# Performance work log

Hardware: AMD Instinct MI355X
Metric: run time of the kernel (lower is better)

Reference implementation:

```python
import jax, jax.numpy as jnp
import numpy as np

B, C, H, W = 8, 192, 64, 64
RED = 8
CR = C // RED  # 24


def prelu(x, a):
    # a is a single shared slope (PyTorch nn.PReLU() default num_parameters=1)
    return jnp.where(x >= 0, x, a * x)


def conv1x1(x, w, b):
    # x: [B,C,H,W], w: [O,C], b: [O] -> [B,O,H,W]
    return jnp.einsum('bchw,oc->bohw', x, w) + b[None, :, None, None]


def setup_inputs() -> dict:
    key = jax.random.key(0)
    ks = jax.random.split(key, 7)
    scale1 = 1.0 / np.sqrt(C)
    return {
        'x': jax.random.normal(ks[0], (B, C, H, W), dtype=jnp.float32),
        'w1': jax.random.uniform(ks[1], (CR, C), jnp.float32, -scale1, scale1),
        'b1': jnp.zeros((CR,), jnp.float32),
        'a1': jnp.full((1,), 0.25, jnp.float32),
        'w2': jax.random.uniform(ks[2], (CR, C), jnp.float32, -scale1, scale1),
        'b2': jnp.zeros((CR,), jnp.float32),
        'a2': jnp.full((1,), 0.25, jnp.float32),
        'wa': jax.random.uniform(ks[3], (C, C), jnp.float32, -scale1, scale1),
        'ba': jnp.zeros((C,), jnp.float32),
        'aa': jnp.full((1,), 0.25, jnp.float32),
    }


def reference(x, w1, b1, a1, w2, b2, a2, wa, ba, aa):
    b, c, h, w = x.shape
    hw = h * w
    q = prelu(conv1x1(x, w1, b1), a1)          # [B,Cr,H,W]
    k = prelu(conv1x1(x, w2, b2), a2)          # [B,Cr,H,W]
    v = prelu(conv1x1(x, wa, ba), aa)          # [B,C,H,W]
    q = q.reshape(b, -1, hw).transpose(0, 2, 1)   # [B,HW,Cr]
    k = k.reshape(b, -1, hw)                      # [B,Cr,HW]
    score = jax.nn.softmax(jnp.einsum('bnc,bcm->bnm', q, k), axis=2)  # [B,HW,HW]
    v = v.reshape(b, c, hw).transpose(0, 2, 1)    # [B,HW,C]
    out = jnp.einsum('bnm,bmc->bnc', score, v)    # [B,HW,C]
    return out.transpose(0, 2, 1).reshape(b, c, h, w)
```

## Files before the change

kernel.cpp:

```cpp
#include <hip/hip_runtime.h>
#include <hip/hip_fp16.h>

#define HW 4096
#define NC 192
#define NB 8
#define DQK 32
#define LOG2E 1.4426950408889634f
#define THRL 11.541560327f

typedef _Float16 f16x8 __attribute__((ext_vector_type(8)));
typedef float f32x4 __attribute__((ext_vector_type(4)));
typedef unsigned int u32x4 __attribute__((ext_vector_type(4)));

#define BAR() do { asm volatile("s_waitcnt lgkmcnt(0)" ::: "memory"); \
                   __builtin_amdgcn_s_barrier();                      \
                   asm volatile("" ::: "memory"); } while (0)

static __device__ __forceinline__ unsigned int pkrtz(float a, float b) {
  auto h = __builtin_amdgcn_cvt_pkrtz(a, b);
  return __builtin_bit_cast(unsigned int, h);
}
static __device__ __forceinline__ unsigned short f2h_bits(float f) {
  _Float16 h = (_Float16)f;
  union { _Float16 h; unsigned short u; } cv; cv.h = h; return cv.u;
}

__global__ void wtrans_kernel(
    const float* __restrict__ w1, const float* __restrict__ b1, const float* __restrict__ a1,
    const float* __restrict__ w2, const float* __restrict__ b2, const float* __restrict__ a2,
    const float* __restrict__ wa, const float* __restrict__ ba, const float* __restrict__ aa,
    float* __restrict__ wt)
{
  const int c = blockIdx.x;
  const int o = threadIdx.x;
  if (o >= 240) return;
  float v;
  if (c < 192) {
    if (o < 24)      v = w1[o * 192 + c];
    else if (o < 48) v = w2[(o - 24) * 192 + c];
    else             v = wa[(o - 48) * 192 + c];
  } else if (c == 192) {
    v = (o < 24) ? b1[o] : (o < 48) ? b2[o - 24] : ba[o - 48];
  } else {
    v = (o < 24) ? a1[0] : (o < 48) ? a2[0] : aa[0];
  }
  wt[c * 240 + o] = v;
}

__global__ __launch_bounds__(256) void proj_kernel(
    const float* __restrict__ x, const float* __restrict__ wt,
    unsigned short* __restrict__ Qn, unsigned short* __restrict__ Kn,
    unsigned short* __restrict__ Vt)
{
  const int g   = blockIdx.y;
  const int tid = threadIdx.x;
  const int bp  = (blockIdx.x * 256 + tid) * 2;
  const int b   = bp >> 12;
  const int pos = bp & (HW - 1);

  const float* xb = x + (size_t)b * NC * HW + pos;
  float acc0[16], acc1[16];
  #pragma unroll
  for (int o = 0; o < 16; ++o) { acc0[o] = 0.f; acc1[o] = 0.f; }

  #pragma unroll 4
  for (int c = 0; c < 192; ++c) {
    float2 xv = *reinterpret_cast<const float2*>(xb + (size_t)c * HW);
    const float* wr = wt + c * 240 + g * 16;
    #pragma unroll
    for (int o = 0; o < 16; ++o) {
      float w = wr[o];
      acc0[o] = fmaf(w, xv.x, acc0[o]);
      acc1[o] = fmaf(w, xv.y, acc1[o]);
    }
  }

  const float* brow = wt + 192 * 240 + g * 16;
  const float* srow = wt + 193 * 240 + g * 16;
  unsigned short h0[16], h1[16];
  #pragma unroll
  for (int o = 0; o < 16; ++o) {
    float bias = brow[o], sm1 = srow[o] - 1.f;
    float v0 = acc0[o] + bias; v0 += fminf(v0, 0.f) * sm1;
    float v1 = acc1[o] + bias; v1 += fminf(v1, 0.f) * sm1;
    if (g * 16 + o < 24) { v0 *= LOG2E; v1 *= LOG2E; }
    h0[o] = f2h_bits(v0);
    h1[o] = f2h_bits(v1);
  }

  if (g >= 3) {
    const int vch0 = g * 16 - 48;
    unsigned int* vp = reinterpret_cast<unsigned int*>(
        Vt + ((size_t)b * NC + vch0) * HW + pos);
    #pragma unroll
    for (int o = 0; o < 16; ++o)
      vp[o * (HW / 2)] = (unsigned int)h0[o] | ((unsigned int)h1[o] << 16);
  } else {
    u32x4 lo0, hi0, lo1, hi1;
    #pragma unroll
    for (int j = 0; j < 4; ++j) {
      lo0[j] = (unsigned int)h0[2 * j] | ((unsigned int)h0[2 * j + 1] << 16);
      hi0[j] = (unsigned int)h0[8 + 2 * j] | ((unsigned int)h0[9 + 2 * j] << 16);
      lo1[j] = (unsigned int)h1[2 * j] | ((unsigned int)h1[2 * j + 1] << 16);
      hi1[j] = (unsigned int)h1[8 + 2 * j] | ((unsigned int)h1[9 + 2 * j] << 16);
    }
    const size_t bpos = (size_t)b * HW + pos;
    if (g == 0) {
      u32x4* q0 = reinterpret_cast<u32x4*>(Qn + bpos * DQK);
      q0[0] = lo0; q0[1] = hi0;
      u32x4* q1 = reinterpret_cast<u32x4*>(Qn + (bpos + 1) * DQK);
      q1[0] = lo1; q1[1] = hi1;
    } else if (g == 1) {
      *reinterpret_cast<u32x4*>(Qn + bpos * DQK + 16) = lo0;
      *reinterpret_cast<u32x4*>(Kn + bpos * DQK) = hi0;
      *reinterpret_cast<u32x4*>(Qn + (bpos + 1) * DQK + 16) = lo1;
      *reinterpret_cast<u32x4*>(Kn + (bpos + 1) * DQK) = hi1;
    } else {
      u32x4* k0 = reinterpret_cast<u32x4*>(Kn + bpos * DQK + 8);
      k0[0] = lo0; k0[1] = hi0;
      u32x4* k1 = reinterpret_cast<u32x4*>(Kn + (bpos + 1) * DQK + 8);
      k1[0] = lo1; k1[1] = hi1;
    }
  }
}

__global__ __launch_bounds__(512, 4) void flash_kernel(
    const unsigned short* __restrict__ Qn, const unsigned short* __restrict__ Kn,
    const unsigned short* __restrict__ Vt, float* __restrict__ out)
{
  const int b    = blockIdx.y;
  const int q0   = blockIdx.x * 64;
  const int tid  = threadIdx.x;
  const int w    = tid >> 6;
  const int half = w >> 2;
  const int wi   = w & 3;
  const int lane = tid & 63;
  const int lq   = lane & 15;
  const int lk   = lane >> 4;

  __shared__ u32x4 Pex[2][2][4][2][64];
  __shared__ float alphaL[2][2][4][16];
  __shared__ float mlL[2][2][64];

  const int mbase = half * (HW / 2);
  const int sigb  = 8 * (lq >> 2) + (lq & 3);

  f16x8 qfrag = *reinterpret_cast<const f16x8*>(
      Qn + ((size_t)b * HW + q0 + 16 * wi + lq) * DQK + 8 * lk);

  float m = -1e30f;
  f32x4 O[12], lacc;
  #pragma unroll
  for (int i = 0; i < 12; ++i) O[i] = (f32x4){0.f, 0.f, 0.f, 0.f};
  lacc = (f32x4){0.f, 0.f, 0.f, 0.f};

  const unsigned short* Kb = Kn + (size_t)b * HW * DQK + (size_t)sigb * DQK + 8 * lk;
  const unsigned short* Vw = Vt + (size_t)b * NC * HW + (size_t)(wi * 48 + lq) * HW + 8 * lk;

  f16x8 vones;
  #pragma unroll
  for (int i = 0; i < 8; ++i) vones[i] = (_Float16)1.0f;

  f16x8 Kf[4];

  auto qk_softmax = [&](int par) {
    f32x4 s[4];
    #pragma unroll
    for (int t = 0; t < 4; ++t)
      s[t] = __builtin_amdgcn_mfma_f32_16x16x32_f16(Kf[t], qfrag,
              (f32x4){0.f, 0.f, 0.f, 0.f}, 0, 0, 0);
    float pmax = s[0][0];
    #pragma unroll
    for (int t = 0; t < 4; ++t)
      #pragma unroll
      for (int r = 0; r < 4; ++r) pmax = fmaxf(pmax, s[t][r]);
    float alpha = 1.f;
    if (__any(pmax > m + THRL)) {
      pmax = fmaxf(pmax, __shfl_xor(pmax, 16));
      pmax = fmaxf(pmax, __shfl_xor(pmax, 32));
      float mn = fmaxf(m, pmax);
      alpha = exp2f(m - mn);
      m = mn;
    }
    float pv[4][4];
    #pragma unroll
    for (int t = 0; t < 4; ++t)
      #pragma unroll
      for (int r = 0; r < 4; ++r) pv[t][r] = exp2f(s[t][r] - m);
    u32x4 pa0, pa1;
    pa0[0] = pkrtz(pv[0][0], pv[0][1]); pa0[1] = pkrtz(pv[0][2], pv[0][3]);
    pa0[2] = pkrtz(pv[2][0], pv[2][1]); pa0[3] = pkrtz(pv[2][2], pv[2][3]);
    pa1[0] = pkrtz(pv[1][0], pv[1][1]); pa1[1] = pkrtz(pv[1][2], pv[1][3]);
    pa1[2] = pkrtz(pv[3][0], pv[3][1]); pa1[3] = pkrtz(pv[3][2], pv[3][3]);
    Pex[par][half][wi][0][lane] = pa0;
    Pex[par][half][wi][1][lane] = pa1;
    if (lane < 16) alphaL[par][half][wi][lane] = alpha;
  };

  #pragma unroll
  for (int t = 0; t < 4; ++t)
    Kf[t] = *reinterpret_cast<const f16x8*>(
        Kb + (size_t)(mbase + 32 * (t & 1) + 4 * (t >> 1)) * DQK);
  qk_softmax(0);
  BAR();

  const int NIT = HW / 2 / 64;
  for (int it = 0; it < NIT; ++it) {
    const int prt = it & 1;
    const bool notlast = (it + 1 < NIT);
    const int m0 = mbase + it * 64;
    const int mnext = m0 + 64;
    if (notlast) {
      #pragma unroll
      for (int t = 0; t < 4; ++t)
        Kf[t] = *reinterpret_cast<const f16x8*>(
            Kb + (size_t)(mnext + 32 * (t & 1) + 4 * (t >> 1)) * DQK);
    }
    #pragma unroll
    for (int tr = 0; tr < 4; ++tr) {
      f32x4 al = *reinterpret_cast<const f32x4*>(&alphaL[prt][half][tr][4 * lk]);
      int diff = (al[0] != 1.f) | (al[1] != 1.f) | (al[2] != 1.f) | (al[3] != 1.f);
      if (__any(diff)) {
        #pragma unroll
        for (int tc = 0; tc < 3; ++tc) {
          O[tr * 3 + tc][0] *= al[0]; O[tr * 3 + tc][1] *= al[1];
          O[tr * 3 + tc][2] *= al[2]; O[tr * 3 + tc][3] *= al[3];
        }
        if (tr == wi) {
          lacc[0] *= al[0]; lacc[1] *= al[1]; lacc[2] *= al[2]; lacc[3] *= al[3];
        }
      }
    }
    {
      f16x8 paf[4];
      #pragma unroll
      for (int tr = 0; tr < 4; ++tr)
        paf[tr] = __builtin_bit_cast(f16x8, Pex[prt][half][tr][0][lane]);
      f16x8 pw = __builtin_bit_cast(f16x8, Pex[prt][half][wi][0][lane]);
      lacc = __builtin_amdgcn_mfma_f32_16x16x32_f16(pw, vones, lacc, 0, 0, 0);
      #pragma unroll
      for (int tc = 0; tc < 3; ++tc) {
        f16x8 vb = *reinterpret_cast<const f16x8*>(
            Vw + (size_t)tc * 16 * HW + m0);
        #pragma unroll
        for (int tr = 0; tr < 4; ++tr)
          O[tr * 3 + tc] = __builtin_amdgcn_mfma_f32_16x16x32_f16(
              paf[tr], vb, O[tr * 3 + tc], 0, 0, 0);
      }
    }
    if (notlast) qk_softmax(prt ^ 1);
    {
      f16x8 paf[4];
      #pragma unroll
      for (int tr = 0; tr < 4; ++tr)
        paf[tr] = __builtin_bit_cast(f16x8, Pex[prt][half][tr][1][lane]);
      f16x8 pw = __builtin_bit_cast(f16x8, Pex[prt][half][wi][1][lane]);
      lacc = __builtin_amdgcn_mfma_f32_16x16x32_f16(pw, vones, lacc, 0, 0, 0);
      #pragma unroll
      for (int tc = 0; tc < 3; ++tc) {
        f16x8 vb = *reinterpret_cast<const f16x8*>(
            Vw + (size_t)tc * 16 * HW + m0 + 32);
        #pragma unroll
        for (int tr = 0; tr < 4; ++tr)
          O[tr * 3 + tc] = __builtin_amdgcn_mfma_f32_16x16x32_f16(
              paf[tr], vb, O[tr * 3 + tc], 0, 0, 0);
      }
    }
    BAR();
  }

  if (lane < 16) mlL[half][0][16 * wi + lane] = m;
  if (lq == 0) {
    #pragma unroll
    for (int r = 0; r < 4; ++r) mlL[half][1][16 * wi + 4 * lk + r] = lacc[r];
  }
  f32x4* Ost = reinterpret_cast<f32x4*>(&Pex[0][0][0][0][0]);
  if (half == 1) {
    #pragma unroll
    for (int i = 0; i < 8; ++i) Ost[(wi * 8 + i) * 64 + lane] = O[i];
  }
  BAR();
  f32x4 f0v[4], f1v[4];
  if (half == 0) {
    #pragma unroll
    for (int tr = 0; tr < 4; ++tr) {
      f32x4 m0v = *reinterpret_cast<const f32x4*>(&mlL[0][0][16 * tr + 4 * lk]);
      f32x4 l0v = *reinterpret_cast<const f32x4*>(&mlL[0][1][16 * tr + 4 * lk]);
      f32x4 m1v = *reinterpret_cast<const f32x4*>(&mlL[1][0][16 * tr + 4 * lk]);
      f32x4 l1v = *reinterpret_cast<const f32x4*>(&mlL[1][1][16 * tr + 4 * lk]);
      #pragma unroll
      for (int r = 0; r < 4; ++r) {
        float M  = fmaxf(m0v[r], m1v[r]);
        float s0 = exp2f(m0v[r] - M), s1 = exp2f(m1v[r] - M);
        float L  = s0 * l0v[r] + s1 * l1v[r];
        f0v[tr][r] = s0 / L; f1v[tr][r] = s1 / L;
      }
    }
    #pragma unroll
    for (int i = 0; i < 8; ++i) {
      const int tr = i / 3, tc = i - tr * 3;
      f32x4 o1 = Ost[(wi * 8 + i) * 64 + lane];
      f32x4 o;
      #pragma unroll
      for (int r = 0; r < 4; ++r) o[r] = O[i][r] * f0v[tr][r] + o1[r] * f1v[tr][r];
      *reinterpret_cast<f32x4*>(
          out + ((size_t)b * NC + wi * 48 + tc * 16 + lq) * HW + q0 + 16 * tr + 4 * lk) = o;
    }
  }
  BAR();
  if (half == 1) {
    #pragma unroll
    for (int i = 0; i < 4; ++i) Ost[(wi * 4 + i) * 64 + lane] = O[8 + i];
  }
  BAR();
  if (half == 0) {
    #pragma unroll
    for (int i = 8; i < 12; ++i) {
      const int tr = i / 3, tc = i - tr * 3;
      f32x4 o1 = Ost[(wi * 4 + (i - 8)) * 64 + lane];
      f32x4 o;
      #pragma unroll
      for (int r = 0; r < 4; ++r) o[r] = O[i][r] * f0v[tr][r] + o1[r] * f1v[tr][r];
      *reinterpret_cast<f32x4*>(
          out + ((size_t)b * NC + wi * 48 + tc * 16 + lq) * HW + q0 + 16 * tr + 4 * lk) = o;
    }
  }
}

extern "C" void kernel_launch(void* const* d_in, const int* in_sizes, int n_in,
                              void* d_out, int out_size, void* d_ws, size_t ws_size,
                              hipStream_t stream) {
  const float* x  = (const float*)d_in[0];
  const float* w1 = (const float*)d_in[1];
  const float* b1 = (const float*)d_in[2];
  const float* a1 = (const float*)d_in[3];
  const float* w2 = (const float*)d_in[4];
  const float* b2 = (const float*)d_in[5];
  const float* a2 = (const float*)d_in[6];
  const float* wa = (const float*)d_in[7];
  const float* ba = (const float*)d_in[8];
  const float* aa = (const float*)d_in[9];
  float* out = (float*)d_out;

  unsigned short* Qn = (unsigned short*)d_ws;
  unsigned short* Kn = Qn + (size_t)NB * HW * DQK;
  unsigned short* Vt = Kn + (size_t)NB * HW * DQK;
  float* wt = out + (out_size - 49152);

  (void)hipMemsetAsync(Qn, 0, (size_t)NB * HW * DQK * 2 * sizeof(unsigned short), stream);

  wtrans_kernel<<<dim3(194), 256, 0, stream>>>(w1, b1, a1, w2, b2, a2, wa, ba, aa, wt);

  dim3 pgrid(HW * NB / 512, 15);
  proj_kernel<<<pgrid, 256, 0, stream>>>(x, wt, Qn, Kn, Vt);

  dim3 fgrid(HW / 64, NB);
  flash_kernel<<<fgrid, 512, 0, stream>>>(Qn, Kn, Vt, out);
}
```

Baseline: 184.0 us.

## Halve flash block query tile and widen per-wave channel span with early V prefetch

Each flash-attention block now covers 32 queries with 256 threads instead of 64 queries with 512. Each wave covers 96 output channels across 2 query row tiles instead of 48 channels across 4, and the batch index is folded into a 1D grid of 1024 blocks. V fragments for the first half of each step are loaded before the K prefetch and rescale, to hide global load latency. The smaller tile gives more blocks for the CUs, but K and V are reused across fewer queries, so memory traffic rises. The projection kernel's position index is switched to a precomputed variable.

After: 363.2 us. 1.97x slower.

```diff
diff --git a/kernel.cpp b/kernel.cpp
--- a/kernel.cpp
+++ b/kernel.cpp
@@ -104,7 +104,7 @@
       lo1[j] = (unsigned int)h1[2 * j] | ((unsigned int)h1[2 * j + 1] << 16);
       hi1[j] = (unsigned int)h1[8 + 2 * j] | ((unsigned int)h1[9 + 2 * j] << 16);
     }
-    const size_t bpos = (size_t)b * HW + pos;
+    const size_t bpos = (size_t)bp;
     if (g == 0) {
       u32x4* q0 = reinterpret_cast<u32x4*>(Qn + bpos * DQK);
       q0[0] = lo0; q0[1] = hi0;
@@ -124,23 +124,23 @@
   }
 }
 
-__global__ __launch_bounds__(512, 4) void flash_kernel(
+__global__ __launch_bounds__(256, 4) void flash_kernel(
     const unsigned short* __restrict__ Qn, const unsigned short* __restrict__ Kn,
     const unsigned short* __restrict__ Vt, float* __restrict__ out)
 {
-  const int b    = blockIdx.y;
-  const int q0   = blockIdx.x * 64;
+  const int b    = blockIdx.x & 7;
+  const int q0   = (blockIdx.x >> 3) * 32;
   const int tid  = threadIdx.x;
   const int w    = tid >> 6;
-  const int half = w >> 2;
-  const int wi   = w & 3;
+  const int half = w >> 1;
+  const int wi   = w & 1;
   const int lane = tid & 63;
   const int lq   = lane & 15;
   const int lk   = lane >> 4;
 
-  __shared__ u32x4 Pex[2][2][4][2][64];
-  __shared__ float alphaL[2][2][4][16];
-  __shared__ float mlL[2][2][64];
+  __shared__ u32x4 Pex[2][2][2][2][64];
+  __shared__ float alphaL[2][2][2][16];
+  __shared__ float mlL[2][2][32];
 
   const int mbase = half * (HW / 2);
   const int sigb  = 8 * (lq >> 2) + (lq & 3);
@@ -155,7 +155,7 @@
   lacc = (f32x4){0.f, 0.f, 0.f, 0.f};
 
   const unsigned short* Kb = Kn + (size_t)b * HW * DQK + (size_t)sigb * DQK + 8 * lk;
-  const unsigned short* Vw = Vt + (size_t)b * NC * HW + (size_t)(wi * 48 + lq) * HW + 8 * lk;
+  const unsigned short* Vw = Vt + (size_t)b * NC * HW + (size_t)(wi * 96 + lq) * HW + 8 * lk;
 
   f16x8 vones;
   #pragma unroll
@@ -210,6 +210,10 @@
     const bool notlast = (it + 1 < NIT);
     const int m0 = mbase + it * 64;
     const int mnext = m0 + 64;
+    f16x8 vb0[6];
+    #pragma unroll
+    for (int tc = 0; tc < 6; ++tc)
+      vb0[tc] = *reinterpret_cast<const f16x8*>(Vw + (size_t)tc * 16 * HW + m0);
     if (notlast) {
       #pragma unroll
       for (int t = 0; t < 4; ++t)
@@ -217,14 +221,14 @@
             Kb + (size_t)(mnext + 32 * (t & 1) + 4 * (t >> 1)) * DQK);
     }
     #pragma unroll
-    for (int tr = 0; tr < 4; ++tr) {
+    for (int tr = 0; tr < 2; ++tr) {
       f32x4 al = *reinterpret_cast<const f32x4*>(&alphaL[prt][half][tr][4 * lk]);
       int diff = (al[0] != 1.f) | (al[1] != 1.f) | (al[2] != 1.f) | (al[3] != 1.f);
       if (__any(diff)) {
         #pragma unroll
-        for (int tc = 0; tc < 3; ++tc) {
-          O[tr * 3 + tc][0] *= al[0]; O[tr * 3 + tc][1] *= al[1];
-          O[tr * 3 + tc][2] *= al[2]; O[tr * 3 + tc][3] *= al[3];
+        for (int tc = 0; tc < 6; ++tc) {
+          O[tr * 6 + tc][0] *= al[0]; O[tr * 6 + tc][1] *= al[1];
+          O[tr * 6 + tc][2] *= al[2]; O[tr * 6 + tc][3] *= al[3];
         }
         if (tr == wi) {
           lacc[0] *= al[0]; lacc[1] *= al[1]; lacc[2] *= al[2]; lacc[3] *= al[3];
@@ -232,38 +236,43 @@
       }
     }
     {
-      f16x8 paf[4];
-      #pragma unroll
-      for (int tr = 0; tr < 4; ++tr)
+      f16x8 paf[2];
+      #pragma unroll
+      for (int tr = 0; tr < 2; ++tr)
         paf[tr] = __builtin_bit_cast(f16x8, Pex[prt][half][tr][0][lane]);
-      f16x8 pw = __builtin_bit_cast(f16x8, Pex[prt][half][wi][0][lane]);
-      lacc = __builtin_amdgcn_mfma_f32_16x16x32_f16(pw, vones, lacc, 0, 0, 0);
-      #pragma unroll
-      for (int tc = 0; tc < 3; ++tc) {
-        f16x8 vb = *reinterpret_cast<const f16x8*>(
-            Vw + (size_t)tc * 16 * HW + m0);
+      lacc = __builtin_amdgcn_mfma_f32_16x16x32_f16(paf[wi], vones, lacc, 0, 0, 0);
+      #pragma unroll
+      for (int tc = 0; tc < 6; ++tc)
         #pragma unroll
-        for (int tr = 0; tr < 4; ++tr)
-          O[tr * 3 + tc] = __builtin_amdgcn_mfma_f32_16x16x32_f16(
-              paf[tr], vb, O[tr * 3 + tc], 0, 0, 0);
-      }
-    }
+        for (int tr = 0; tr < 2; ++tr)
+          O[tr * 6 + tc] = __builtin_amdgcn_mfma_f32_16x16x32_f16(
+              paf[tr], vb0[tc], O[tr * 6 + tc], 0, 0, 0);
+    }
+    f16x8 vb1a[3];
+    #pragma unroll
+    for (int tc = 0; tc < 3; ++tc)
+      vb1a[tc] = *reinterpret_cast<const f16x8*>(Vw + (size_t)tc * 16 * HW + m0 + 32);
     if (notlast) qk_softmax(prt ^ 1);
     {
-      f16x8 paf[4];
-      #pragma unroll
-      for (int tr = 0; tr < 4; ++tr)
+      f16x8 paf[2];
+      #pragma unroll
+      for (int tr = 0; tr < 2; ++tr)
         paf[tr] = __builtin_bit_cast(f16x8, Pex[prt][half][tr][1][lane]);
-      f16x8 pw = __builtin_bit_cast(f16x8, Pex[prt][half][wi][1][lane]);
-      lacc = __builtin_amdgcn_mfma_f32_16x16x32_f16(pw, vones, lacc, 0, 0, 0);
-      #pragma unroll
-      for (int tc = 0; tc < 3; ++tc) {
+      lacc = __builtin_amdgcn_mfma_f32_16x16x32_f16(paf[wi], vones, lacc, 0, 0, 0);
+      #pragma unroll
+      for (int tc = 0; tc < 3; ++tc)
+        #pragma unroll
+        for (int tr = 0; tr < 2; ++tr)
+          O[tr * 6 + tc] = __builtin_amdgcn_mfma_f32_16x16x32_f16(
+              paf[tr], vb1a[tc], O[tr * 6 + tc], 0, 0, 0);
+      #pragma unroll
+      for (int tc = 3; tc < 6; ++tc) {
         f16x8 vb = *reinterpret_cast<const f16x8*>(
             Vw + (size_t)tc * 16 * HW + m0 + 32);
         #pragma unroll
-        for (int tr = 0; tr < 4; ++tr)
-          O[tr * 3 + tc] = __builtin_amdgcn_mfma_f32_16x16x32_f16(
-              paf[tr], vb, O[tr * 3 + tc], 0, 0, 0);
+        for (int tr = 0; tr < 2; ++tr)
+          O[tr * 6 + tc] = __builtin_amdgcn_mfma_f32_16x16x32_f16(
+              paf[tr], vb, O[tr * 6 + tc], 0, 0, 0);
       }
     }
     BAR();
@@ -277,13 +286,13 @@
   f32x4* Ost = reinterpret_cast<f32x4*>(&Pex[0][0][0][0][0]);
   if (half == 1) {
     #pragma unroll
-    for (int i = 0; i < 8; ++i) Ost[(wi * 8 + i) * 64 + lane] = O[i];
+    for (int i = 0; i < 6; ++i) Ost[(wi * 6 + i) * 64 + lane] = O[i];
   }
   BAR();
-  f32x4 f0v[4], f1v[4];
+  f32x4 f0v[2], f1v[2];
   if (half == 0) {
     #pragma unroll
-    for (int tr = 0; tr < 4; ++tr) {
+    for (int tr = 0; tr < 2; ++tr) {
       f32x4 m0v = *reinterpret_cast<const f32x4*>(&mlL[0][0][16 * tr + 4 * lk]);
       f32x4 l0v = *reinterpret_cast<const f32x4*>(&mlL[0][1][16 * tr + 4 * lk]);
       f32x4 m1v = *reinterpret_cast<const f32x4*>(&mlL[1][0][16 * tr + 4 * lk]);
@@ -297,32 +306,30 @@
       }
     }
     #pragma unroll
-    for (int i = 0; i < 8; ++i) {
-      const int tr = i / 3, tc = i - tr * 3;
-      f32x4 o1 = Ost[(wi * 8 + i) * 64 + lane];
+    for (int i = 0; i < 6; ++i) {
+      f32x4 o1 = Ost[(wi * 6 + i) * 64 + lane];
       f32x4 o;
       #pragma unroll
-      for (int r = 0; r < 4; ++r) o[r] = O[i][r] * f0v[tr][r] + o1[r] * f1v[tr][r];
+      for (int r = 0; r < 4; ++r) o[r] = O[i][r] * f0v[0][r] + o1[r] * f1v[0][r];
       *reinterpret_cast<f32x4*>(
-          out + ((size_t)b * NC + wi * 48 + tc * 16 + lq) * HW + q0 + 16 * tr + 4 * lk) = o;
+          out + ((size_t)b * NC + wi * 96 + i * 16 + lq) * HW + q0 + 4 * lk) = o;
     }
   }
   BAR();
   if (half == 1) {
     #pragma unroll
-    for (int i = 0; i < 4; ++i) Ost[(wi * 4 + i) * 64 + lane] = O[8 + i];
+    for (int i = 0; i < 6; ++i) Ost[(wi * 6 + i) * 64 + lane] = O[6 + i];
   }
   BAR();
   if (half == 0) {
     #pragma unroll
-    for (int i = 8; i < 12; ++i) {
-      const int tr = i / 3, tc = i - tr * 3;
-      f32x4 o1 = Ost[(wi * 4 + (i - 8)) * 64 + lane];
+    for (int i = 0; i < 6; ++i) {
+      f32x4 o1 = Ost[(wi * 6 + i) * 64 + lane];
       f32x4 o;
       #pragma unroll
-      for (int r = 0; r < 4; ++r) o[r] = O[i][r] * f0v[tr][r] + o1[r] * f1v[tr][r];
+      for (int r = 0; r < 4; ++r) o[r] = O[6 + i][r] * f0v[1][r] + o1[r] * f1v[1][r];
       *reinterpret_cast<f32x4*>(
-          out + ((size_t)b * NC + wi * 48 + tc * 16 + lq) * HW + q0 + 16 * tr + 4 * lk) = o;
+          out + ((size_t)b * NC + wi * 96 + i * 16 + lq) * HW + q0 + 16 + 4 * lk) = o;
     }
   }
 }
@@ -354,6 +361,5 @@
   dim3 pgrid(HW * NB / 512, 15);
   proj_kernel<<<pgrid, 256, 0, stream>>>(x, wt, Qn, Kn, Vt);
 
-  dim3 fgrid(HW / 64, NB);
-  flash_kernel<<<fgrid, 512, 0, stream>>>(Qn, Kn, Vt, out);
-}
+  flash_kernel<<<dim3(1024), 256, 0, stream>>>(Qn, Kn, Vt, out);
+}
```

## Drop intra-block KV split in flash kernel, use 256-thread blocks with V prefetch

Applied to the files above, without the earlier changes.

The flash kernel previously split the key range across two half-blocks of 4 waves each and merged their partial (m, l, O) results through shared memory at the end. Now each 256-thread block of 4 waves walks the full key range, so the cross-half merge and the extra barriers go away, and V fragments are loaded earlier in each iteration so their latency overlaps other work. The trade-off is half as many waves per query tile, which means less parallelism per block and a longer serial loop per wave. The proj kernel also switches to a precomputed bp index for the Q/K store address.

New measurement: 492.8 us. +167.9%, slower.

```diff
diff --git a/kernel.cpp b/kernel.cpp
--- a/kernel.cpp
+++ b/kernel.cpp
@@ -104,7 +104,7 @@
       lo1[j] = (unsigned int)h1[2 * j] | ((unsigned int)h1[2 * j + 1] << 16);
       hi1[j] = (unsigned int)h1[8 + 2 * j] | ((unsigned int)h1[9 + 2 * j] << 16);
     }
-    const size_t bpos = (size_t)b * HW + pos;
+    const size_t bpos = (size_t)bp;
     if (g == 0) {
       u32x4* q0 = reinterpret_cast<u32x4*>(Qn + bpos * DQK);
       q0[0] = lo0; q0[1] = hi0;
@@ -124,26 +124,23 @@
   }
 }
 
-__global__ __launch_bounds__(512, 4) void flash_kernel(
+__global__ __launch_bounds__(256, 4) void flash_kernel(
     const unsigned short* __restrict__ Qn, const unsigned short* __restrict__ Kn,
     const unsigned short* __restrict__ Vt, float* __restrict__ out)
 {
   const int b    = blockIdx.y;
   const int q0   = blockIdx.x * 64;
   const int tid  = threadIdx.x;
-  const int w    = tid >> 6;
-  const int half = w >> 2;
-  const int wi   = w & 3;
+  const int wi   = tid >> 6;
   const int lane = tid & 63;
   const int lq   = lane & 15;
   const int lk   = lane >> 4;
 
-  __shared__ u32x4 Pex[2][2][4][2][64];
-  __shared__ float alphaL[2][2][4][16];
-  __shared__ float mlL[2][2][64];
-
-  const int mbase = half * (HW / 2);
-  const int sigb  = 8 * (lq >> 2) + (lq & 3);
+  __shared__ u32x4 Pex[2][4][2][64];
+  __shared__ float alphaL[2][4][16];
+  __shared__ float lL[64];
+
+  const int sigb = 8 * (lq >> 2) + (lq & 3);
 
   f16x8 qfrag = *reinterpret_cast<const f16x8*>(
       Qn + ((size_t)b * HW + q0 + 16 * wi + lq) * DQK + 8 * lk);
@@ -192,24 +189,28 @@
     pa0[2] = pkrtz(pv[2][0], pv[2][1]); pa0[3] = pkrtz(pv[2][2], pv[2][3]);
     pa1[0] = pkrtz(pv[1][0], pv[1][1]); pa1[1] = pkrtz(pv[1][2], pv[1][3]);
     pa1[2] = pkrtz(pv[3][0], pv[3][1]); pa1[3] = pkrtz(pv[3][2], pv[3][3]);
-    Pex[par][half][wi][0][lane] = pa0;
-    Pex[par][half][wi][1][lane] = pa1;
-    if (lane < 16) alphaL[par][half][wi][lane] = alpha;
+    Pex[par][wi][0][lane] = pa0;
+    Pex[par][wi][1][lane] = pa1;
+    if (lane < 16) alphaL[par][wi][lane] = alpha;
   };
 
   #pragma unroll
   for (int t = 0; t < 4; ++t)
     Kf[t] = *reinterpret_cast<const f16x8*>(
-        Kb + (size_t)(mbase + 32 * (t & 1) + 4 * (t >> 1)) * DQK);
+        Kb + (size_t)(32 * (t & 1) + 4 * (t >> 1)) * DQK);
   qk_softmax(0);
   BAR();
 
-  const int NIT = HW / 2 / 64;
+  const int NIT = HW / 64;
   for (int it = 0; it < NIT; ++it) {
     const int prt = it & 1;
     const bool notlast = (it + 1 < NIT);
-    const int m0 = mbase + it * 64;
+    const int m0 = it * 64;
     const int mnext = m0 + 64;
+    f16x8 vb0[3];
+    #pragma unroll
+    for (int tc = 0; tc < 3; ++tc)
+      vb0[tc] = *reinterpret_cast<const f16x8*>(Vw + (size_t)tc * 16 * HW + m0);
     if (notlast) {
       #pragma unroll
       for (int t = 0; t < 4; ++t)
@@ -218,7 +219,7 @@
     }
     #pragma unroll
     for (int tr = 0; tr < 4; ++tr) {
-      f32x4 al = *reinterpret_cast<const f32x4*>(&alphaL[prt][half][tr][4 * lk]);
+      f32x4 al = *reinterpret_cast<const f32x4*>(&alphaL[prt][tr][4 * lk]);
       int diff = (al[0] != 1.f) | (al[1] != 1.f) | (al[2] != 1.f) | (al[3] != 1.f);
       if (__any(diff)) {
         #pragma unroll
@@ -235,92 +236,52 @@
       f16x8 paf[4];
       #pragma unroll
       for (int tr = 0; tr < 4; ++tr)
-        paf[tr] = __builtin_bit_cast(f16x8, Pex[prt][half][tr][0][lane]);
-      f16x8 pw = __builtin_bit_cast(f16x8, Pex[prt][half][wi][0][lane]);
-      lacc = __builtin_amdgcn_mfma_f32_16x16x32_f16(pw, vones, lacc, 0, 0, 0);
-      #pragma unroll
-      for (int tc = 0; tc < 3; ++tc) {
-        f16x8 vb = *reinterpret_cast<const f16x8*>(
-            Vw + (size_t)tc * 16 * HW + m0);
+        paf[tr] = __builtin_bit_cast(f16x8, Pex[prt][tr][0][lane]);
+      lacc = __builtin_amdgcn_mfma_f32_16x16x32_f16(paf[wi], vones, lacc, 0, 0, 0);
+      #pragma unroll
+      for (int tc = 0; tc < 3; ++tc)
         #pragma unroll
         for (int tr = 0; tr < 4; ++tr)
           O[tr * 3 + tc] = __builtin_amdgcn_mfma_f32_16x16x32_f16(
-              paf[tr], vb, O[tr * 3 + tc], 0, 0, 0);
-      }
-    }
+              paf[tr], vb0[tc], O[tr * 3 + tc], 0, 0, 0);
+    }
+    f16x8 vb1[3];
+    #pragma unroll
+    for (int tc = 0; tc < 3; ++tc)
+      vb1[tc] = *reinterpret_cast<const f16x8*>(Vw + (size_t)tc * 16 * HW + m0 + 32);
     if (notlast) qk_softmax(prt ^ 1);
     {
       f16x8 paf[4];
       #pragma unroll
       for (int tr = 0; tr < 4; ++tr)
-        paf[tr] = __builtin_bit_cast(f16x8, Pex[prt][half][tr][1][lane]);
-      f16x8 pw = __builtin_bit_cast(f16x8, Pex[prt][half][wi][1][lane]);
-      lacc = __builtin_amdgcn_mfma_f32_16x16x32_f16(pw, vones, lacc, 0, 0, 0);
-      #pragma unroll
-      for (int tc = 0; tc < 3; ++tc) {
-        f16x8 vb = *reinterpret_cast<const f16x8*>(
-            Vw + (size_t)tc * 16 * HW + m0 + 32);
+        paf[tr] = __builtin_bit_cast(f16x8, Pex[prt][tr][1][lane]);
+      lacc = __builtin_amdgcn_mfma_f32_16x16x32_f16(paf[wi], vones, lacc, 0, 0, 0);
+      #pragma unroll
+      for (int tc = 0; tc < 3; ++tc)
         #pragma unroll
         for (int tr = 0; tr < 4; ++tr)
           O[tr * 3 + tc] = __builtin_amdgcn_mfma_f32_16x16x32_f16(
-              paf[tr], vb, O[tr * 3 + tc], 0, 0, 0);
-      }
+              paf[tr], vb1[tc], O[tr * 3 + tc], 0, 0, 0);
     }
     BAR();
   }
 
-  if (lane < 16) mlL[half][0][16 * wi + lane] = m;
   if (lq == 0) {
     #pragma unroll
-    for (int r = 0; r < 4; ++r) mlL[half][1][16 * wi + 4 * lk + r] = lacc[r];
-  }
-  f32x4* Ost = reinterpret_cast<f32x4*>(&Pex[0][0][0][0][0]);
-  if (half == 1) {
-    #pragma unroll
-    for (int i = 0; i < 8; ++i) Ost[(wi * 8 + i) * 64 + lane] = O[i];
+    for (int r = 0; r < 4; ++r) lL[16 * wi + 4 * lk + r] = lacc[r];
   }
   BAR();
-  f32x4 f0v[4], f1v[4];
-  if (half == 0) {
-    #pragma unroll
-    for (int tr = 0; tr < 4; ++tr) {
-      f32x4 m0v = *reinterpret_cast<const f32x4*>(&mlL[0][0][16 * tr + 4 * lk]);
-      f32x4 l0v = *reinterpret_cast<const f32x4*>(&mlL[0][1][16 * tr + 4 * lk]);
-      f32x4 m1v = *reinterpret_cast<const f32x4*>(&mlL[1][0][16 * tr + 4 * lk]);
-      f32x4 l1v = *reinterpret_cast<const f32x4*>(&mlL[1][1][16 * tr + 4 * lk]);
-      #pragma unroll
-      for (int r = 0; r < 4; ++r) {
-        float M  = fmaxf(m0v[r], m1v[r]);
-        float s0 = exp2f(m0v[r] - M), s1 = exp2f(m1v[r] - M);
-        float L  = s0 * l0v[r] + s1 * l1v[r];
-        f0v[tr][r] = s0 / L; f1v[tr][r] = s1 / L;
-      }
-    }
-    #pragma unroll
-    for (int i = 0; i < 8; ++i) {
-      const int tr = i / 3, tc = i - tr * 3;
-      f32x4 o1 = Ost[(wi * 8 + i) * 64 + lane];
+  #pragma unroll
+  for (int tr = 0; tr < 4; ++tr) {
+    f32x4 lv = *reinterpret_cast<const f32x4*>(&lL[16 * tr + 4 * lk]);
+    f32x4 inv;
+    #pragma unroll
+    for (int r = 0; r < 4; ++r) inv[r] = 1.f / lv[r];
+    #pragma unroll
+    for (int tc = 0; tc < 3; ++tc) {
       f32x4 o;
       #pragma unroll
-      for (int r = 0; r < 4; ++r) o[r] = O[i][r] * f0v[tr][r] + o1[r] * f1v[tr][r];
-      *reinterpret_cast<f32x4*>(
-          out + ((size_t)b * NC + wi * 48 + tc * 16 + lq) * HW + q0 + 16 * tr + 4 * lk) = o;
-    }
-  }
-  BAR();
-  if (half == 1) {
-    #pragma unroll
-    for (int i = 0; i < 4; ++i) Ost[(wi * 4 + i) * 64 + lane] = O[8 + i];
-  }
-  BAR();
-  if (half == 0) {
-    #pragma unroll
-    for (int i = 8; i < 12; ++i) {
-      const int tr = i / 3, tc = i - tr * 3;
-      f32x4 o1 = Ost[(wi * 4 + (i - 8)) * 64 + lane];
-      f32x4 o;
-      #pragma unroll
-      for (int r = 0; r < 4; ++r) o[r] = O[i][r] * f0v[tr][r] + o1[r] * f1v[tr][r];
+      for (int r = 0; r < 4; ++r) o[r] = O[tr * 3 + tc][r] * inv[r];
       *reinterpret_cast<f32x4*>(
           out + ((size_t)b * NC + wi * 48 + tc * 16 + lq) * HW + q0 + 16 * tr + 4 * lk) = o;
     }
@@ -355,5 +316,5 @@
   proj_kernel<<<pgrid, 256, 0, stream>>>(x, wt, Qn, Kn, Vt);
 
   dim3 fgrid(HW / 64, NB);
-  flash_kernel<<<fgrid, 512, 0, stream>>>(Qn, Kn, Vt, out);
-}
+  flash_kernel<<<fgrid, 256, 0, stream>>>(Qn, Kn, Vt, out);
+}
```

## Hoist V/P loads ahead of MFMA and gate rescaling with per-wave flag bytes

Applied to the files above, without the earlier changes.

Each wave now writes a per-wave byte flag in shared memory recording whether its running max changed. It writes alpha values only when that flag is set. The consumer reads one packed flag word to skip the alpha reads and O rescaling when nothing changed, instead of reading four alpha vectors and voting. The P fragments and V loads for both halves are issued earlier so their latency overlaps K loads and the softmax. The prologue also switches to a precomputed bp index. Risks are higher register pressure from holding the prefetched fragments and a possible undefined `bp`, which is not visible in the shown code.

After: 402.3 us. 119% more time.

```diff
diff --git a/kernel.cpp b/kernel.cpp
--- a/kernel.cpp
+++ b/kernel.cpp
@@ -104,7 +104,7 @@
       lo1[j] = (unsigned int)h1[2 * j] | ((unsigned int)h1[2 * j + 1] << 16);
       hi1[j] = (unsigned int)h1[8 + 2 * j] | ((unsigned int)h1[9 + 2 * j] << 16);
     }
-    const size_t bpos = (size_t)b * HW + pos;
+    const size_t bpos = (size_t)bp;
     if (g == 0) {
       u32x4* q0 = reinterpret_cast<u32x4*>(Qn + bpos * DQK);
       q0[0] = lo0; q0[1] = hi0;
@@ -141,6 +141,7 @@
   __shared__ u32x4 Pex[2][2][4][2][64];
   __shared__ float alphaL[2][2][4][16];
   __shared__ float mlL[2][2][64];
+  __shared__ unsigned int aflag[2][2];
 
   const int mbase = half * (HW / 2);
   const int sigb  = 8 * (lq >> 2) + (lq & 3);
@@ -175,7 +176,8 @@
       #pragma unroll
       for (int r = 0; r < 4; ++r) pmax = fmaxf(pmax, s[t][r]);
     float alpha = 1.f;
-    if (__any(pmax > m + THRL)) {
+    const bool trig = __any(pmax > m + THRL);
+    if (trig) {
       pmax = fmaxf(pmax, __shfl_xor(pmax, 16));
       pmax = fmaxf(pmax, __shfl_xor(pmax, 32));
       float mn = fmaxf(m, pmax);
@@ -194,7 +196,10 @@
     pa1[2] = pkrtz(pv[3][0], pv[3][1]); pa1[3] = pkrtz(pv[3][2], pv[3][3]);
     Pex[par][half][wi][0][lane] = pa0;
     Pex[par][half][wi][1][lane] = pa1;
-    if (lane < 16) alphaL[par][half][wi][lane] = alpha;
+    if (lane == 0)
+      ((unsigned char*)&aflag[par][half])[wi] = trig ? 1u : 0u;
+    if (trig && lane < 16)
+      alphaL[par][half][wi][lane] = alpha;
   };
 
   #pragma unroll
@@ -210,61 +215,63 @@
     const bool notlast = (it + 1 < NIT);
     const int m0 = mbase + it * 64;
     const int mnext = m0 + 64;
+    f16x8 paf0[4];
+    #pragma unroll
+    for (int tr = 0; tr < 4; ++tr)
+      paf0[tr] = __builtin_bit_cast(f16x8, Pex[prt][half][tr][0][lane]);
+    f16x8 vb0[3];
+    #pragma unroll
+    for (int tc = 0; tc < 3; ++tc)
+      vb0[tc] = *reinterpret_cast<const f16x8*>(Vw + (size_t)tc * 16 * HW + m0);
     if (notlast) {
       #pragma unroll
       for (int t = 0; t < 4; ++t)
         Kf[t] = *reinterpret_cast<const f16x8*>(
             Kb + (size_t)(mnext + 32 * (t & 1) + 4 * (t >> 1)) * DQK);
     }
-    #pragma unroll
-    for (int tr = 0; tr < 4; ++tr) {
-      f32x4 al = *reinterpret_cast<const f32x4*>(&alphaL[prt][half][tr][4 * lk]);
-      int diff = (al[0] != 1.f) | (al[1] != 1.f) | (al[2] != 1.f) | (al[3] != 1.f);
-      if (__any(diff)) {
-        #pragma unroll
-        for (int tc = 0; tc < 3; ++tc) {
-          O[tr * 3 + tc][0] *= al[0]; O[tr * 3 + tc][1] *= al[1];
-          O[tr * 3 + tc][2] *= al[2]; O[tr * 3 + tc][3] *= al[3];
-        }
-        if (tr == wi) {
-          lacc[0] *= al[0]; lacc[1] *= al[1]; lacc[2] *= al[2]; lacc[3] *= al[3];
+    const unsigned int fl = aflag[prt][half];
+    if (fl) {
+      #pragma unroll
+      for (int tr = 0; tr < 4; ++tr) {
+        if (fl & (0xffu << (8 * tr))) {
+          f32x4 al = *reinterpret_cast<const f32x4*>(&alphaL[prt][half][tr][4 * lk]);
+          #pragma unroll
+          for (int tc = 0; tc < 3; ++tc) {
+            O[tr * 3 + tc][0] *= al[0]; O[tr * 3 + tc][1] *= al[1];
+            O[tr * 3 + tc][2] *= al[2]; O[tr * 3 + tc][3] *= al[3];
+          }
+          if (tr == wi) {
+            lacc[0] *= al[0]; lacc[1] *= al[1]; lacc[2] *= al[2]; lacc[3] *= al[3];
+          }
         }
       }
     }
     {
-      f16x8 paf[4];
-      #pragma unroll
-      for (int tr = 0; tr < 4; ++tr)
-        paf[tr] = __builtin_bit_cast(f16x8, Pex[prt][half][tr][0][lane]);
-      f16x8 pw = __builtin_bit_cast(f16x8, Pex[prt][half][wi][0][lane]);
-      lacc = __builtin_amdgcn_mfma_f32_16x16x32_f16(pw, vones, lacc, 0, 0, 0);
-      #pragma unroll
-      for (int tc = 0; tc < 3; ++tc) {
-        f16x8 vb = *reinterpret_cast<const f16x8*>(
-            Vw + (size_t)tc * 16 * HW + m0);
+      lacc = __builtin_amdgcn_mfma_f32_16x16x32_f16(paf0[wi], vones, lacc, 0, 0, 0);
+      #pragma unroll
+      for (int tc = 0; tc < 3; ++tc)
         #pragma unroll
         for (int tr = 0; tr < 4; ++tr)
           O[tr * 3 + tc] = __builtin_amdgcn_mfma_f32_16x16x32_f16(
-              paf[tr], vb, O[tr * 3 + tc], 0, 0, 0);
-      }
-    }
+              paf0[tr], vb0[tc], O[tr * 3 + tc], 0, 0, 0);
+    }
+    f16x8 vb1[3];
+    #pragma unroll
+    for (int tc = 0; tc < 3; ++tc)
+      vb1[tc] = *reinterpret_cast<const f16x8*>(Vw + (size_t)tc * 16 * HW + m0 + 32);
     if (notlast) qk_softmax(prt ^ 1);
     {
-      f16x8 paf[4];
+      f16x8 paf1[4];
       #pragma unroll
       for (int tr = 0; tr < 4; ++tr)
-        paf[tr] = __builtin_bit_cast(f16x8, Pex[prt][half][tr][1][lane]);
-      f16x8 pw = __builtin_bit_cast(f16x8, Pex[prt][half][wi][1][lane]);
-      lacc = __builtin_amdgcn_mfma_f32_16x16x32_f16(pw, vones, lacc, 0, 0, 0);
-      #pragma unroll
-      for (int tc = 0; tc < 3; ++tc) {
-        f16x8 vb = *reinterpret_cast<const f16x8*>(
-            Vw + (size_t)tc * 16 * HW + m0 + 32);
+        paf1[tr] = __builtin_bit_cast(f16x8, Pex[prt][half][tr][1][lane]);
+      lacc = __builtin_amdgcn_mfma_f32_16x16x32_f16(paf1[wi], vones, lacc, 0, 0, 0);
+      #pragma unroll
+      for (int tc = 0; tc < 3; ++tc)
         #pragma unroll
         for (int tr = 0; tr < 4; ++tr)
           O[tr * 3 + tc] = __builtin_amdgcn_mfma_f32_16x16x32_f16(
-              paf[tr], vb, O[tr * 3 + tc], 0, 0, 0);
-      }
+              paf1[tr], vb1[tc], O[tr * 3 + tc], 0, 0, 0);
     }
     BAR();
   }
```
